# Optimization experiments

Measured on AMD Instinct MI355X. Metric: run time of the kernel, lower is better.

## Reference

```python
import jax, jax.numpy as jnp
import numpy as np
import math

L, D, H, FF = 6, 512, 8, 2048
B, S = 8, 1024
EPS = 1e-5


def sin_pos_embedding(num_embeddings, dim, padding_idx=0):
    half = dim // 2
    freq = jnp.exp(jnp.arange(half, dtype=jnp.float32) * (-math.log(10000.0) / (half - 1)))
    ang = jnp.arange(num_embeddings, dtype=jnp.float32)[:, None] * freq[None, :]
    emb = jnp.concatenate([jnp.sin(ang), jnp.cos(ang)], axis=1)
    return emb.at[padding_idx].set(0.0)


def layer_norm(x, g, b):
    mu = jnp.mean(x, axis=-1, keepdims=True)
    var = jnp.mean(jnp.square(x - mu), axis=-1, keepdims=True)
    return (x - mu) * jax.lax.rsqrt(var + EPS) * g + b


def setup_inputs() -> dict:
    key = jax.random.key(0)
    ks = jax.random.split(key, 16)
    s = 0.02
    inp = {
        'x': jax.random.normal(ks[0], (B, S, D), jnp.float32),
        'char_ids': jax.random.randint(ks[1], (B, S), 0, 10000, jnp.int64) if jax.config.read('jax_enable_x64') else jax.random.randint(ks[1], (B, S), 0, 10000, jnp.int32),
        'seq_len': jnp.full((B,), S, jnp.int32),
        'mask': jnp.ones((B, S), jnp.int32),
        'Wqkv': jax.random.normal(ks[2], (L, D, 3 * D), jnp.float32) * s,
        'Wfc': jax.random.normal(ks[3], (L, D, D), jnp.float32) * s,
        'bfc': jnp.zeros((L, D), jnp.float32),
        'ln1_g': jnp.ones((L, D), jnp.float32), 'ln1_b': jnp.zeros((L, D), jnp.float32),
        'ln2_g': jnp.ones((L, D), jnp.float32), 'ln2_b': jnp.zeros((L, D), jnp.float32),
        'W1': jax.random.normal(ks[4], (L, D, FF), jnp.float32) * s,
        'b1': jnp.zeros((L, FF), jnp.float32),
        'W2': jax.random.normal(ks[5], (L, FF, D), jnp.float32) * s,
        'b2': jnp.zeros((L, D), jnp.float32),
    }
    return inp


def reference(x, char_ids, seq_len, mask, Wqkv, Wfc, bfc, ln1_g, ln1_b, ln2_g, ln2_b, W1, b1, W2, b2):
    # sinusoidal positional embedding computed from mask positions (padding_idx=0)
    valid = (mask != 0).astype(jnp.int32)
    positions = jnp.cumsum(valid, axis=1) * valid  # [B,S], pads -> 0
    table = sin_pos_embedding(S + 2, D)  # max_pos = padding_idx+1+S
    x = x + table[positions]

    key_mask = (mask == 0)[:, None, None, :]  # [B,1,1,S]
    dh = D // H

    for l in range(L):
        residual = x
        qkv = jnp.einsum('bsd,de->bse', x, Wqkv[l])  # [B,S,3D]
        q, k, v = jnp.split(qkv, 3, axis=-1)
        q = q.reshape(B, S, H, dh).transpose(0, 2, 1, 3)  # [B,H,S,dh]
        k = k.reshape(B, S, H, dh).transpose(0, 2, 1, 3)
        v = v.reshape(B, S, H, dh).transpose(0, 2, 1, 3)
        attn = jnp.einsum('bhqd,bhkd->bhqk', q, k)  # scale=1 (scale=False)
        attn = jnp.where(key_mask, -jnp.inf, attn)
        attn = jax.nn.softmax(attn, axis=-1)
        o = jnp.einsum('bhqk,bhkd->bhqd', attn, v)
        o = o.transpose(0, 2, 1, 3).reshape(B, S, D)
        o = jnp.einsum('bsd,de->bse', o, Wfc[l]) + bfc[l]
        x = layer_norm(o + residual, ln1_g[l], ln1_b[l])
        residual = x
        h = jax.nn.relu(jnp.einsum('bsd,df->bsf', x, W1[l]) + b1[l])
        h = jnp.einsum('bsf,fd->bsd', h, W2[l]) + b2[l]
        x = layer_norm(residual + h, ln2_g[l], ln2_b[l])
    return x
```

## Files before the change

### kernel.cpp

```cpp
#include <hip/hip_runtime.h>
#include <math.h>

#define LAYERS 6
#define DMODEL 512
#define NHEAD 8
#define DHEAD 64
#define FFDIM 2048
#define BATCH 8
#define SEQ 1024
#define ROWS (BATCH * SEQ)
#define EPS 1e-5f

typedef __attribute__((ext_vector_type(8))) short bf16x8;
typedef __attribute__((ext_vector_type(4))) float f32x4;

__device__ inline short f2bf(float f) {
    union { float f; unsigned u; } v; v.f = f;
    unsigned r = (v.u + 0x7FFFu + ((v.u >> 16) & 1u)) >> 16;
    return (short)r;
}

#define GLOAD_LDS16(g, l)                                                      \
    __builtin_amdgcn_global_load_lds(                                          \
        (__attribute__((address_space(1))) void*)(g),                          \
        (__attribute__((address_space(3))) void*)(l), 16, 0, 0)

__global__ void wtrans_kernel(const float* __restrict__ src, short* __restrict__ dst,
                              int K, int N) {
    __shared__ float t[32][33];
    const size_t mofs = (size_t)blockIdx.z * K * N;
    src += mofs; dst += mofs;
    int n0 = blockIdx.x * 32, k0 = blockIdx.y * 32;
    int tx = threadIdx.x, ty = threadIdx.y;
#pragma unroll
    for (int i = 0; i < 4; ++i)
        t[ty + 8 * i][tx] = src[(size_t)(k0 + ty + 8 * i) * N + n0 + tx];
    __syncthreads();
#pragma unroll
    for (int i = 0; i < 4; ++i)
        dst[(size_t)(n0 + ty + 8 * i) * K + k0 + tx] = f2bf(t[tx][ty + 8 * i]);
}

__global__ void pos_scan_kernel(const int* __restrict__ mask, int* __restrict__ pos) {
    __shared__ int sm[SEQ];
    int b = blockIdx.x;
    int t = threadIdx.x;
    int v = (mask[b * SEQ + t] != 0) ? 1 : 0;
    sm[t] = v;
    __syncthreads();
    for (int off = 1; off < SEQ; off <<= 1) {
        int add = (t >= off) ? sm[t - off] : 0;
        __syncthreads();
        sm[t] += add;
        __syncthreads();
    }
    pos[b * SEQ + t] = sm[t] * v;
}

__global__ void add_pos_kernel(const float* __restrict__ xin, const int* __restrict__ pos,
                               float* __restrict__ xout, short* __restrict__ xb) {
    int bs = blockIdx.x;
    int t = threadIdx.x;
    int p = pos[bs];
    int d0 = t * 4;
    const float C = -logf(10000.0f) * (1.0f / 255.0f);
    float4 xv = *(const float4*)(xin + (size_t)bs * DMODEL + d0);
    float e[4];
#pragma unroll
    for (int j = 0; j < 4; ++j) {
        int d = d0 + j;
        if (p == 0) {
            e[j] = 0.0f;
        } else {
            int dd = (d < 256) ? d : d - 256;
            float freq = expf((float)dd * C);
            float ang = (float)p * freq;
            e[j] = (d < 256) ? sinf(ang) : cosf(ang);
        }
    }
    float4 ov;
    ov.x = xv.x + e[0]; ov.y = xv.y + e[1]; ov.z = xv.z + e[2]; ov.w = xv.w + e[3];
    *(float4*)(xout + (size_t)bs * DMODEL + d0) = ov;
    short4 sb;
    sb.x = f2bf(ov.x); sb.y = f2bf(ov.y); sb.z = f2bf(ov.z); sb.w = f2bf(ov.w);
    *(short4*)(xb + (size_t)bs * DMODEL + d0) = sb;
}


template <bool OUTBF16, bool BIAS, bool RELU>
__global__ __launch_bounds__(256) void gemm_bf16_kernel(const short* __restrict__ A,
                                                        const short* __restrict__ BT,
                                                        const float* __restrict__ bias,
                                                        void* __restrict__ Cv,
                                                        int M, int N, int K) {
    __shared__ __attribute__((aligned(16))) short Asm[2][128 * 32];
    __shared__ __attribute__((aligned(16))) short Bsm[2][128 * 32];
    const int tid = threadIdx.x;
    const int w = tid >> 6;
    const int lane = tid & 63;
    const int quad = lane >> 4;
    const int lr = lane & 15;
    const int m0 = blockIdx.y * 128;
    const int n0 = blockIdx.x * 128;
    const int wm = (w >> 1) * 64;
    const int wn = (w & 1) * 64;

    const int segr = lane >> 2;
    const int segk = (((lane & 3) - (lane >> 3)) & 3) * 8;
    const int sA0 = w * 2, sA1 = w * 2 + 1;
    const short* gA0 = A + (size_t)(m0 + sA0 * 16 + segr) * K + segk;
    const short* gA1 = A + (size_t)(m0 + sA1 * 16 + segr) * K + segk;
    const short* gB0 = BT + (size_t)(n0 + sA0 * 16 + segr) * K + segk;
    const short* gB1 = BT + (size_t)(n0 + sA1 * 16 + segr) * K + segk;
    const int lofs0 = sA0 * 512 + lane * 8;
    const int lofs1 = sA1 * 512 + lane * 8;
    const int gp = ((quad + (lr >> 1)) & 3) * 8;

    f32x4 acc[4][4];
#pragma unroll
    for (int i = 0; i < 4; ++i)
#pragma unroll
        for (int j = 0; j < 4; ++j) { acc[i][j][0] = 0.f; acc[i][j][1] = 0.f; acc[i][j][2] = 0.f; acc[i][j][3] = 0.f; }

    GLOAD_LDS16(gA0, &Asm[0][lofs0]);
    GLOAD_LDS16(gA1, &Asm[0][lofs1]);
    GLOAD_LDS16(gB0, &Bsm[0][lofs0]);
    GLOAD_LDS16(gB1, &Bsm[0][lofs1]);

    const int nk = K >> 5;
    for (int i = 0; i < nk; ++i) {
        __syncthreads();
        if (i + 1 < nk) {
            const int k1 = (i + 1) * 32;
            const int nb = (i + 1) & 1;
            GLOAD_LDS16(gA0 + k1, &Asm[nb][lofs0]);
            GLOAD_LDS16(gA1 + k1, &Asm[nb][lofs1]);
            GLOAD_LDS16(gB0 + k1, &Bsm[nb][lofs0]);
            GLOAD_LDS16(gB1 + k1, &Bsm[nb][lofs1]);
        }
        const int cur = i & 1;
        bf16x8 af[4], bfr[4];
#pragma unroll
        for (int mt = 0; mt < 4; ++mt)
            af[mt] = *(const bf16x8*)&Asm[cur][(wm + mt * 16 + lr) * 32 + gp];
#pragma unroll
        for (int nt = 0; nt < 4; ++nt)
            bfr[nt] = *(const bf16x8*)&Bsm[cur][(wn + nt * 16 + lr) * 32 + gp];
#pragma unroll
        for (int mt = 0; mt < 4; ++mt)
#pragma unroll
            for (int nt = 0; nt < 4; ++nt)
                acc[mt][nt] = __builtin_amdgcn_mfma_f32_16x16x32_bf16(af[mt], bfr[nt], acc[mt][nt], 0, 0, 0);
    }

    float bv[4];
    if (BIAS) {
#pragma unroll
        for (int nt = 0; nt < 4; ++nt) bv[nt] = bias[n0 + wn + nt * 16 + lr];
    }
#pragma unroll
    for (int mt = 0; mt < 4; ++mt)
#pragma unroll
        for (int nt = 0; nt < 4; ++nt)
#pragma unroll
            for (int r = 0; r < 4; ++r) {
                float v = acc[mt][nt][r];
                if (BIAS) v += bv[nt];
                if (RELU) v = fmaxf(v, 0.f);
                int row = m0 + wm + mt * 16 + quad * 4 + r;
                int col = n0 + wn + nt * 16 + lr;
                if (OUTBF16)
                    ((short*)Cv)[(size_t)row * N + col] = f2bf(v);
                else
                    ((float*)Cv)[(size_t)row * N + col] = v;
            }
}

template <bool OUTBF16, bool BIAS, bool RELU>
__global__ __launch_bounds__(256) void gemm_bf16_m64_kernel(const short* __restrict__ A,
                                                            const short* __restrict__ BT,
                                                            const float* __restrict__ bias,
                                                            void* __restrict__ Cv,
                                                            int M, int N, int K) {
    __shared__ __attribute__((aligned(16))) short Asm[2][64 * 32];
    __shared__ __attribute__((aligned(16))) short Bsm[2][128 * 32];
    const int tid = threadIdx.x;
    const int w = tid >> 6;
    const int lane = tid & 63;
    const int quad = lane >> 4;
    const int lr = lane & 15;
    const int m0 = blockIdx.y * 64;
    const int n0 = blockIdx.x * 128;
    const int wm = (w >> 1) * 32;
    const int wn = (w & 1) * 64;

    const int segr = lane >> 2;
    const int segk = (((lane & 3) - (lane >> 3)) & 3) * 8;
    const short* gA  = A + (size_t)(m0 + w * 16 + segr) * K + segk;
    const short* gB0 = BT + (size_t)(n0 + (2 * w) * 16 + segr) * K + segk;
    const short* gB1 = BT + (size_t)(n0 + (2 * w + 1) * 16 + segr) * K + segk;
    const int lA  = w * 512 + lane * 8;
    const int lB0 = (2 * w) * 512 + lane * 8;
    const int lB1 = (2 * w + 1) * 512 + lane * 8;
    const int gp = ((quad + (lr >> 1)) & 3) * 8;

    f32x4 acc[2][4];
#pragma unroll
    for (int i = 0; i < 2; ++i)
#pragma unroll
        for (int j = 0; j < 4; ++j) { acc[i][j][0] = 0.f; acc[i][j][1] = 0.f; acc[i][j][2] = 0.f; acc[i][j][3] = 0.f; }

    GLOAD_LDS16(gA, &Asm[0][lA]);
    GLOAD_LDS16(gB0, &Bsm[0][lB0]);
    GLOAD_LDS16(gB1, &Bsm[0][lB1]);

    const int nk = K >> 5;
    for (int i = 0; i < nk; ++i) {
        __syncthreads();
        if (i + 1 < nk) {
            const int k1 = (i + 1) * 32;
            const int nb = (i + 1) & 1;
            GLOAD_LDS16(gA + k1, &Asm[nb][lA]);
            GLOAD_LDS16(gB0 + k1, &Bsm[nb][lB0]);
            GLOAD_LDS16(gB1 + k1, &Bsm[nb][lB1]);
        }
        const int cur = i & 1;
        bf16x8 af[2], bfr[4];
#pragma unroll
        for (int mt = 0; mt < 2; ++mt)
            af[mt] = *(const bf16x8*)&Asm[cur][(wm + mt * 16 + lr) * 32 + gp];
#pragma unroll
        for (int nt = 0; nt < 4; ++nt)
            bfr[nt] = *(const bf16x8*)&Bsm[cur][(wn + nt * 16 + lr) * 32 + gp];
#pragma unroll
        for (int mt = 0; mt < 2; ++mt)
#pragma unroll
            for (int nt = 0; nt < 4; ++nt)
                acc[mt][nt] = __builtin_amdgcn_mfma_f32_16x16x32_bf16(af[mt], bfr[nt], acc[mt][nt], 0, 0, 0);
    }

    float bv[4];
    if (BIAS) {
#pragma unroll
        for (int nt = 0; nt < 4; ++nt) bv[nt] = bias[n0 + wn + nt * 16 + lr];
    }
#pragma unroll
    for (int mt = 0; mt < 2; ++mt)
#pragma unroll
        for (int nt = 0; nt < 4; ++nt)
#pragma unroll
            for (int r = 0; r < 4; ++r) {
                float v = acc[mt][nt][r];
                if (BIAS) v += bv[nt];
                if (RELU) v = fmaxf(v, 0.f);
                int row = m0 + wm + mt * 16 + quad * 4 + r;
                int col = n0 + wn + nt * 16 + lr;
                if (OUTBF16)
                    ((short*)Cv)[(size_t)row * N + col] = f2bf(v);
                else
                    ((float*)Cv)[(size_t)row * N + col] = v;
            }
}

#define QTILE 128
__global__ __launch_bounds__(512, 4) void attn_mfma_kernel(const short* __restrict__ qkv,
                                                           const int* __restrict__ mask,
                                                           short* __restrict__ o) {
    __shared__ __attribute__((aligned(16))) short Ks[2][64][72];
    __shared__ __attribute__((aligned(16))) short Vt[2][64][72];
    __shared__ __attribute__((aligned(16))) short Ps[8][16][72];
    __shared__ float Msf[2][64];

    const int qt = blockIdx.x;
    const int bh = blockIdx.y;
    const int b = bh >> 3, h = bh & 7;
    const int tid = threadIdx.x;
    const int w = tid >> 6;
    const int lane = tid & 63;
    const int quad = lane >> 4;
    const int lr = lane & 15;
    const size_t seqrow = (size_t)b * SEQ;

    bf16x8 qf[2];
#pragma unroll
    for (int c = 0; c < 2; ++c)
        qf[c] = *(const bf16x8*)(qkv +
            (seqrow + qt * QTILE + w * 16 + lr) * (3 * DMODEL)
            + h * DHEAD + c * 32 + quad * 8);

    const bool isK = (tid < 256);
    const int st = isK ? tid : tid - 256;
    const int kkey = st >> 2;
    const int kg = (st & 3) * 8;
    const int vkp = st & 31;
    const int vdg = st >> 5;
    const short* gK = qkv + (seqrow + kkey) * (3 * DMODEL) + DMODEL + h * DHEAD + kg;
    const short* gV = qkv + (seqrow + 2 * vkp) * (3 * DMODEL) + 2 * DMODEL + h * DHEAD + vdg * 8;

    bf16x8 r0, r1;
    int mreg = 0;

    {
        if (isK) {
            r0 = *(const bf16x8*)(gK);
            r1 = *(const bf16x8*)(gK + 32);
        } else {
            r0 = *(const bf16x8*)(gV);
            r1 = *(const bf16x8*)(gV + 3 * DMODEL);
        }
        if (tid < 64) mreg = mask[seqrow + tid];
        if (isK) {
            *(bf16x8*)&Ks[0][kkey][kg] = r0;
            *(bf16x8*)&Ks[0][kkey][kg + 32] = r1;
        } else {
#pragma unroll
            for (int i = 0; i < 8; ++i) {
                short2 p; p.x = r0[i]; p.y = r1[i];
                *(short2*)&Vt[0][vdg * 8 + i][vkp * 2] = p;
            }
        }
        if (tid < 64) Msf[0][tid] = mreg ? 1.0f : 0.0f;
    }
    __syncthreads();

    f32x4 Oacc[4];
    float rs = 0.f;
#pragma unroll
    for (int t2 = 0; t2 < 4; ++t2) { Oacc[t2][0] = 0.f; Oacc[t2][1] = 0.f; Oacc[t2][2] = 0.f; Oacc[t2][3] = 0.f; }

    for (int kt = 0; kt < 16; ++kt) {
        const int cur = kt & 1;
        {
            const size_t ofs = (size_t)((kt + 1) & 15) * 64 * (3 * DMODEL);
            if (isK) {
                r0 = *(const bf16x8*)(gK + ofs);
                r1 = *(const bf16x8*)(gK + ofs + 32);
            } else {
                r0 = *(const bf16x8*)(gV + ofs);
                r1 = *(const bf16x8*)(gV + ofs + 3 * DMODEL);
            }
            if (tid < 64) mreg = mask[seqrow + ((kt + 1) & 15) * 64 + tid];
        }
        bf16x8 kf[2][4], vf[2][4];
#pragma unroll
        for (int c = 0; c < 2; ++c)
#pragma unroll
            for (int t = 0; t < 4; ++t) {
                kf[c][t] = *(const bf16x8*)&Ks[cur][lr + 16 * t][quad * 8 + 32 * c];
                vf[c][t] = *(const bf16x8*)&Vt[cur][lr + 16 * t][quad * 8 + 32 * c];
            }

        f32x4 S[4];
#pragma unroll
        for (int t = 0; t < 4; ++t) { S[t][0] = 0.f; S[t][1] = 0.f; S[t][2] = 0.f; S[t][3] = 0.f; }
#pragma unroll
        for (int c = 0; c < 2; ++c)
#pragma unroll
            for (int t = 0; t < 4; ++t)
                S[t] = __builtin_amdgcn_mfma_f32_16x16x32_bf16(kf[c][t], qf[c], S[t], 0, 0, 0);

#pragma unroll
        for (int t = 0; t < 4; ++t) {
            f32x4 mvv = *(const f32x4*)&Msf[cur][16 * t + 4 * quad];
            float p0 = __expf(S[t][0] - 8.0f) * mvv[0];
            float p1 = __expf(S[t][1] - 8.0f) * mvv[1];
            float p2 = __expf(S[t][2] - 8.0f) * mvv[2];
            float p3 = __expf(S[t][3] - 8.0f) * mvv[3];
            rs += (p0 + p1) + (p2 + p3);
            unsigned lo, hi;
            asm("v_cvt_pk_bf16_f32 %0, %1, %2" : "=v"(lo) : "v"(p0), "v"(p1));
            asm("v_cvt_pk_bf16_f32 %0, %1, %2" : "=v"(hi) : "v"(p2), "v"(p3));
            uint2 pk; pk.x = lo; pk.y = hi;
            *(uint2*)&Ps[w][lr][16 * t + 4 * quad] = pk;
        }
        bf16x8 pa0 = *(const bf16x8*)&Ps[w][lr][quad * 8];
        bf16x8 pa1 = *(const bf16x8*)&Ps[w][lr][quad * 8 + 32];
#pragma unroll
        for (int t2 = 0; t2 < 4; ++t2) {
            Oacc[t2] = __builtin_amdgcn_mfma_f32_16x16x32_bf16(pa0, vf[0][t2], Oacc[t2], 0, 0, 0);
            Oacc[t2] = __builtin_amdgcn_mfma_f32_16x16x32_bf16(pa1, vf[1][t2], Oacc[t2], 0, 0, 0);
        }

        {
            const int nb = cur ^ 1;
            if (isK) {
                *(bf16x8*)&Ks[nb][kkey][kg] = r0;
                *(bf16x8*)&Ks[nb][kkey][kg + 32] = r1;
            } else {
#pragma unroll
                for (int i = 0; i < 8; ++i) {
                    short2 p; p.x = r0[i]; p.y = r1[i];
                    *(short2*)&Vt[nb][vdg * 8 + i][vkp * 2] = p;
                }
            }
            if (tid < 64) Msf[nb][tid] = mreg ? 1.0f : 0.0f;
        }
        __syncthreads();
    }

    rs += __shfl_xor(rs, 16);
    rs += __shfl_xor(rs, 32);
    float inv[4];
#pragma unroll
    for (int r = 0; r < 4; ++r)
        inv[r] = 1.f / __shfl(rs, quad * 4 + r);

#pragma unroll
    for (int t2 = 0; t2 < 4; ++t2)
#pragma unroll
        for (int r = 0; r < 4; ++r) {
            int row = qt * QTILE + w * 16 + quad * 4 + r;
            o[(seqrow + row) * DMODEL + h * DHEAD + 16 * t2 + lr] = f2bf(Oacc[t2][r] * inv[r]);
        }
}

__global__ __launch_bounds__(64) void ln_kernel(const float* __restrict__ tmp,
                                                float* __restrict__ x,
                                                short* __restrict__ xb,
                                                const float* __restrict__ g,
                                                const float* __restrict__ bta) {
    const int row = blockIdx.x;
    const int t = threadIdx.x;
    const size_t base = (size_t)row * DMODEL + t * 8;
    float4 x0 = *(const float4*)(x + base);
    float4 x1 = *(const float4*)(x + base + 4);
    float4 t0 = *(const float4*)(tmp + base);
    float4 t1 = *(const float4*)(tmp + base + 4);
    float v[8];
    v[0] = x0.x + t0.x; v[1] = x0.y + t0.y; v[2] = x0.z + t0.z; v[3] = x0.w + t0.w;
    v[4] = x1.x + t1.x; v[5] = x1.y + t1.y; v[6] = x1.z + t1.z; v[7] = x1.w + t1.w;
    float s = 0.f, sq = 0.f;
#pragma unroll
    for (int i = 0; i < 8; ++i) { s += v[i]; sq += v[i] * v[i]; }
#pragma unroll
    for (int off = 1; off < 64; off <<= 1) {
        s += __shfl_xor(s, off);
        sq += __shfl_xor(sq, off);
    }
    float mu = s * (1.0f / DMODEL);
    float var = sq * (1.0f / DMODEL) - mu * mu;
    float r = rsqrtf(var + EPS);
    float4 g0 = *(const float4*)(g + t * 8);
    float4 g1 = *(const float4*)(g + t * 8 + 4);
    float4 b0 = *(const float4*)(bta + t * 8);
    float4 b1 = *(const float4*)(bta + t * 8 + 4);
    float ov[8];
    ov[0] = (v[0] - mu) * r * g0.x + b0.x;
    ov[1] = (v[1] - mu) * r * g0.y + b0.y;
    ov[2] = (v[2] - mu) * r * g0.z + b0.z;
    ov[3] = (v[3] - mu) * r * g0.w + b0.w;
    ov[4] = (v[4] - mu) * r * g1.x + b1.x;
    ov[5] = (v[5] - mu) * r * g1.y + b1.y;
    ov[6] = (v[6] - mu) * r * g1.z + b1.z;
    ov[7] = (v[7] - mu) * r * g1.w + b1.w;
    *(float4*)(x + base) = *(float4*)&ov[0];
    *(float4*)(x + base + 4) = *(float4*)&ov[4];
    bf16x8 ob;
#pragma unroll
    for (int i = 0; i < 8; ++i) ob[i] = f2bf(ov[i]);
    *(bf16x8*)(xb + base) = ob;
}

extern "C" void kernel_launch(void* const* d_in, const int* in_sizes, int n_in,
                              void* d_out, int out_size, void* d_ws, size_t ws_size,
                              hipStream_t stream) {
    const float* x_in  = (const float*)d_in[0];
    const int*   mask  = (const int*)d_in[3];
    const float* Wqkv  = (const float*)d_in[4];
    const float* Wfc   = (const float*)d_in[5];
    const float* bfc   = (const float*)d_in[6];
    const float* ln1_g = (const float*)d_in[7];
    const float* ln1_b = (const float*)d_in[8];
    const float* ln2_g = (const float*)d_in[9];
    const float* ln2_b = (const float*)d_in[10];
    const float* W1    = (const float*)d_in[11];
    const float* b1    = (const float*)d_in[12];
    const float* W2    = (const float*)d_in[13];
    const float* b2    = (const float*)d_in[14];

    float* x = (float*)d_out;

    char* ws = (char*)d_ws;
    size_t ofs = 0;
    int*   pos   = (int*)ws;                 ofs += 65536;
    float* tmp   = (float*)(ws + ofs);       ofs += (size_t)ROWS * DMODEL * 4;
    short* xb    = (short*)(ws + ofs);       ofs += (size_t)ROWS * DMODEL * 2;
    short* qkvb  = (short*)(ws + ofs);
    short* hb    = (short*)(ws + ofs);
    ofs += (size_t)ROWS * 3 * DMODEL * 2;
    short* obuf  = (short*)(ws + ofs);       ofs += (size_t)ROWS * DMODEL * 2;
    short* WqkvT = (short*)(ws + ofs);       ofs += (size_t)LAYERS * DMODEL * 3 * DMODEL * 2;
    short* WfcT  = (short*)(ws + ofs);       ofs += (size_t)LAYERS * DMODEL * DMODEL * 2;
    short* W1T   = (short*)(ws + ofs);       ofs += (size_t)LAYERS * DMODEL * FFDIM * 2;
    short* W2T   = (short*)(ws + ofs);       ofs += (size_t)LAYERS * FFDIM * DMODEL * 2;

    wtrans_kernel<<<dim3(3 * DMODEL / 32, DMODEL / 32, LAYERS), dim3(32, 8), 0, stream>>>(
        Wqkv, WqkvT, DMODEL, 3 * DMODEL);
    wtrans_kernel<<<dim3(DMODEL / 32, DMODEL / 32, LAYERS), dim3(32, 8), 0, stream>>>(
        Wfc, WfcT, DMODEL, DMODEL);
    wtrans_kernel<<<dim3(FFDIM / 32, DMODEL / 32, LAYERS), dim3(32, 8), 0, stream>>>(
        W1, W1T, DMODEL, FFDIM);
    wtrans_kernel<<<dim3(DMODEL / 32, FFDIM / 32, LAYERS), dim3(32, 8), 0, stream>>>(
        W2, W2T, FFDIM, DMODEL);

    pos_scan_kernel<<<BATCH, SEQ, 0, stream>>>(mask, pos);
    add_pos_kernel<<<ROWS, 128, 0, stream>>>(x_in, pos, x, xb);

    for (int l = 0; l < LAYERS; ++l) {
        const short* wqkvT_l = WqkvT + (size_t)l * DMODEL * 3 * DMODEL;
        const short* wfcT_l  = WfcT + (size_t)l * DMODEL * DMODEL;
        const short* w1T_l   = W1T + (size_t)l * DMODEL * FFDIM;
        const short* w2T_l   = W2T + (size_t)l * FFDIM * DMODEL;
        const float* bfc_l   = bfc + (size_t)l * DMODEL;
        const float* b1_l    = b1 + (size_t)l * FFDIM;
        const float* b2_l    = b2 + (size_t)l * DMODEL;

        gemm_bf16_kernel<true, false, false><<<dim3(3 * DMODEL / 128, ROWS / 128), 256, 0, stream>>>(
            xb, wqkvT_l, nullptr, qkvb, ROWS, 3 * DMODEL, DMODEL);
        attn_mfma_kernel<<<dim3(SEQ / QTILE, BATCH * NHEAD), 512, 0, stream>>>(qkvb, mask, obuf);
        gemm_bf16_m64_kernel<false, true, false><<<dim3(DMODEL / 128, ROWS / 64), 256, 0, stream>>>(
            obuf, wfcT_l, bfc_l, tmp, ROWS, DMODEL, DMODEL);
        ln_kernel<<<ROWS, 64, 0, stream>>>(tmp, x, xb, ln1_g + (size_t)l * DMODEL,
                                           ln1_b + (size_t)l * DMODEL);
        gemm_bf16_kernel<true, true, true><<<dim3(FFDIM / 128, ROWS / 128), 256, 0, stream>>>(
            xb, w1T_l, b1_l, hb, ROWS, FFDIM, DMODEL);
        gemm_bf16_m64_kernel<false, true, false><<<dim3(DMODEL / 128, ROWS / 64), 256, 0, stream>>>(
            hb, w2T_l, b2_l, tmp, ROWS, DMODEL, FFDIM);
        ln_kernel<<<ROWS, 64, 0, stream>>>(tmp, x, xb, ln2_g + (size_t)l * DMODEL,
                                           ln2_b + (size_t)l * DMODEL);
    }
}
```

Baseline: 1.096 ms.

## Switch attention to 32x32x16 MFMA with register-shuffled P and 256-row query tiles

Rewrites the attention kernel to use 32x32x16 bf16 MFMA instructions, with each wave handling 32 query rows and the query tile doubled to 256. The softmax probabilities are rearranged into the A-operand layout through cross-lane shuffles instead of a round trip through shared memory, which removes the Ps LDS buffer. Each K/V tile loaded into LDS is now reused across twice as many query rows. In exchange, registers per thread rise and occupancy drops (launch bounds go from 4 to 2 blocks), and the grid has half as many blocks.

New measurement: 1.091 ms. Within noise of the previous version (-0.4%).

```diff
diff --git a/kernel.cpp b/kernel.cpp
--- a/kernel.cpp
+++ b/kernel.cpp
@@ -13,6 +13,7 @@
 
 typedef __attribute__((ext_vector_type(8))) short bf16x8;
 typedef __attribute__((ext_vector_type(4))) float f32x4;
+typedef __attribute__((ext_vector_type(16))) float f32x16;
 
 __device__ inline short f2bf(float f) {
     union { float f; unsigned u; } v; v.f = f;
@@ -262,14 +263,13 @@
             }
 }
 
-#define QTILE 128
-__global__ __launch_bounds__(512, 4) void attn_mfma_kernel(const short* __restrict__ qkv,
+#define QTILE 256
+__global__ __launch_bounds__(512, 2) void attn_mfma_kernel(const short* __restrict__ qkv,
                                                            const int* __restrict__ mask,
                                                            short* __restrict__ o) {
     __shared__ __attribute__((aligned(16))) short Ks[2][64][72];
     __shared__ __attribute__((aligned(16))) short Vt[2][64][72];
-    __shared__ __attribute__((aligned(16))) short Ps[8][16][72];
-    __shared__ float Msf[2][64];
+    __shared__ __attribute__((aligned(16))) float Msf[2][64];
 
     const int qt = blockIdx.x;
     const int bh = blockIdx.y;
@@ -277,16 +277,16 @@
     const int tid = threadIdx.x;
     const int w = tid >> 6;
     const int lane = tid & 63;
-    const int quad = lane >> 4;
-    const int lr = lane & 15;
+    const int c31 = lane & 31;
+    const int hi = lane >> 5;
     const size_t seqrow = (size_t)b * SEQ;
 
-    bf16x8 qf[2];
-#pragma unroll
-    for (int c = 0; c < 2; ++c)
-        qf[c] = *(const bf16x8*)(qkv +
-            (seqrow + qt * QTILE + w * 16 + lr) * (3 * DMODEL)
-            + h * DHEAD + c * 32 + quad * 8);
+    bf16x8 qf[4];
+#pragma unroll
+    for (int ks = 0; ks < 4; ++ks)
+        qf[ks] = *(const bf16x8*)(qkv +
+            (seqrow + qt * QTILE + w * 32 + c31) * (3 * DMODEL)
+            + h * DHEAD + ks * 16 + hi * 8);
 
     const bool isK = (tid < 256);
     const int st = isK ? tid : tid - 256;
@@ -323,10 +323,10 @@
     }
     __syncthreads();
 
-    f32x4 Oacc[4];
+    f32x16 O0, O1;
     float rs = 0.f;
 #pragma unroll
-    for (int t2 = 0; t2 < 4; ++t2) { Oacc[t2][0] = 0.f; Oacc[t2][1] = 0.f; Oacc[t2][2] = 0.f; Oacc[t2][3] = 0.f; }
+    for (int i = 0; i < 16; ++i) { O0[i] = 0.f; O1[i] = 0.f; }
 
     for (int kt = 0; kt < 16; ++kt) {
         const int cur = kt & 1;
@@ -341,44 +341,55 @@
             }
             if (tid < 64) mreg = mask[seqrow + ((kt + 1) & 15) * 64 + tid];
         }
-        bf16x8 kf[2][4], vf[2][4];
-#pragma unroll
-        for (int c = 0; c < 2; ++c)
-#pragma unroll
-            for (int t = 0; t < 4; ++t) {
-                kf[c][t] = *(const bf16x8*)&Ks[cur][lr + 16 * t][quad * 8 + 32 * c];
-                vf[c][t] = *(const bf16x8*)&Vt[cur][lr + 16 * t][quad * 8 + 32 * c];
+
+        f32x16 S0, S1;
+#pragma unroll
+        for (int i = 0; i < 16; ++i) { S0[i] = 0.f; S1[i] = 0.f; }
+#pragma unroll
+        for (int ks = 0; ks < 4; ++ks) {
+            bf16x8 k0 = *(const bf16x8*)&Ks[cur][c31][ks * 16 + hi * 8];
+            bf16x8 k1 = *(const bf16x8*)&Ks[cur][32 + c31][ks * 16 + hi * 8];
+            S0 = __builtin_amdgcn_mfma_f32_32x32x16_bf16(k0, qf[ks], S0, 0, 0, 0);
+            S1 = __builtin_amdgcn_mfma_f32_32x32x16_bf16(k1, qf[ks], S1, 0, 0, 0);
+        }
+
+        unsigned pkd[2][8];
+#pragma unroll
+        for (int g = 0; g < 4; ++g) {
+            f32x4 m0 = *(const f32x4*)&Msf[cur][g * 8 + hi * 4];
+            f32x4 m1 = *(const f32x4*)&Msf[cur][32 + g * 8 + hi * 4];
+            float p0[4], p1[4];
+#pragma unroll
+            for (int j = 0; j < 4; ++j) {
+                p0[j] = __expf(S0[g * 4 + j] - 8.0f) * m0[j];
+                p1[j] = __expf(S1[g * 4 + j] - 8.0f) * m1[j];
+                rs += p0[j] + p1[j];
             }
-
-        f32x4 S[4];
-#pragma unroll
-        for (int t = 0; t < 4; ++t) { S[t][0] = 0.f; S[t][1] = 0.f; S[t][2] = 0.f; S[t][3] = 0.f; }
-#pragma unroll
-        for (int c = 0; c < 2; ++c)
-#pragma unroll
-            for (int t = 0; t < 4; ++t)
-                S[t] = __builtin_amdgcn_mfma_f32_16x16x32_bf16(kf[c][t], qf[c], S[t], 0, 0, 0);
-
-#pragma unroll
-        for (int t = 0; t < 4; ++t) {
-            f32x4 mvv = *(const f32x4*)&Msf[cur][16 * t + 4 * quad];
-            float p0 = __expf(S[t][0] - 8.0f) * mvv[0];
-            float p1 = __expf(S[t][1] - 8.0f) * mvv[1];
-            float p2 = __expf(S[t][2] - 8.0f) * mvv[2];
-            float p3 = __expf(S[t][3] - 8.0f) * mvv[3];
-            rs += (p0 + p1) + (p2 + p3);
-            unsigned lo, hi;
-            asm("v_cvt_pk_bf16_f32 %0, %1, %2" : "=v"(lo) : "v"(p0), "v"(p1));
-            asm("v_cvt_pk_bf16_f32 %0, %1, %2" : "=v"(hi) : "v"(p2), "v"(p3));
-            uint2 pk; pk.x = lo; pk.y = hi;
-            *(uint2*)&Ps[w][lr][16 * t + 4 * quad] = pk;
-        }
-        bf16x8 pa0 = *(const bf16x8*)&Ps[w][lr][quad * 8];
-        bf16x8 pa1 = *(const bf16x8*)&Ps[w][lr][quad * 8 + 32];
-#pragma unroll
-        for (int t2 = 0; t2 < 4; ++t2) {
-            Oacc[t2] = __builtin_amdgcn_mfma_f32_16x16x32_bf16(pa0, vf[0][t2], Oacc[t2], 0, 0, 0);
-            Oacc[t2] = __builtin_amdgcn_mfma_f32_16x16x32_bf16(pa1, vf[1][t2], Oacc[t2], 0, 0, 0);
+            asm("v_cvt_pk_bf16_f32 %0, %1, %2" : "=v"(pkd[0][g * 2])     : "v"(p0[0]), "v"(p0[1]));
+            asm("v_cvt_pk_bf16_f32 %0, %1, %2" : "=v"(pkd[0][g * 2 + 1]) : "v"(p0[2]), "v"(p0[3]));
+            asm("v_cvt_pk_bf16_f32 %0, %1, %2" : "=v"(pkd[1][g * 2])     : "v"(p1[0]), "v"(p1[1]));
+            asm("v_cvt_pk_bf16_f32 %0, %1, %2" : "=v"(pkd[1][g * 2 + 1]) : "v"(p1[2]), "v"(p1[3]));
+        }
+
+#pragma unroll
+        for (int ks = 0; ks < 4; ++ks) {
+            const int k2 = ks >> 1;
+            const int i0 = (ks & 1) * 4;
+            unsigned c0a = pkd[k2][i0 + 0], c0b = pkd[k2][i0 + 1];
+            unsigned c1a = pkd[k2][i0 + 2], c1b = pkd[k2][i0 + 3];
+            unsigned x1a = (unsigned)__shfl_xor((int)c1a, 32);
+            unsigned x1b = (unsigned)__shfl_xor((int)c1b, 32);
+            unsigned x0a = (unsigned)__shfl_xor((int)c0a, 32);
+            unsigned x0b = (unsigned)__shfl_xor((int)c0b, 32);
+            union { unsigned u[4]; bf16x8 v; } pb;
+            pb.u[0] = hi ? x1a : c0a;
+            pb.u[1] = hi ? x1b : c0b;
+            pb.u[2] = hi ? c1a : x0a;
+            pb.u[3] = hi ? c1b : x0b;
+            bf16x8 v0 = *(const bf16x8*)&Vt[cur][c31][ks * 16 + hi * 8];
+            bf16x8 v1 = *(const bf16x8*)&Vt[cur][32 + c31][ks * 16 + hi * 8];
+            O0 = __builtin_amdgcn_mfma_f32_32x32x16_bf16(pb.v, v0, O0, 0, 0, 0);
+            O1 = __builtin_amdgcn_mfma_f32_32x32x16_bf16(pb.v, v1, O1, 0, 0, 0);
         }
 
         {
@@ -398,20 +409,16 @@
         __syncthreads();
     }
 
-    rs += __shfl_xor(rs, 16);
     rs += __shfl_xor(rs, 32);
-    float inv[4];
-#pragma unroll
-    for (int r = 0; r < 4; ++r)
-        inv[r] = 1.f / __shfl(rs, quad * 4 + r);
-
-#pragma unroll
-    for (int t2 = 0; t2 < 4; ++t2)
-#pragma unroll
-        for (int r = 0; r < 4; ++r) {
-            int row = qt * QTILE + w * 16 + quad * 4 + r;
-            o[(seqrow + row) * DMODEL + h * DHEAD + 16 * t2 + lr] = f2bf(Oacc[t2][r] * inv[r]);
-        }
+
+#pragma unroll
+    for (int r = 0; r < 16; ++r) {
+        const int qr = (r & 3) + 8 * (r >> 2) + 4 * hi;
+        const float inv = 1.0f / __shfl(rs, qr);
+        const int row = qt * QTILE + w * 32 + qr;
+        o[(seqrow + row) * DMODEL + h * DHEAD + c31]      = f2bf(O0[r] * inv);
+        o[(seqrow + row) * DMODEL + h * DHEAD + 32 + c31] = f2bf(O1[r] * inv);
+    }
 }
 
 __global__ __launch_bounds__(64) void ln_kernel(const float* __restrict__ tmp,
```
